# Kernel tuning notes

Hardware: AMD Instinct MI355X
Metric: run time of the kernel (lower is better)

## Reference

```python
import jax, jax.numpy as jnp
import numpy as np

N, E, D_IN, D_H, D_OUT = 100000, 1600000, 128, 128, 47
BN_EPS = 1e-5


def setup_inputs() -> dict:
    key = jax.random.key(0)
    ks = jax.random.split(key, 12)
    x = jax.random.normal(ks[0], (N, D_IN), dtype=jnp.float32)
    edge_index = jax.random.randint(ks[1], (2, E), 0, N, dtype=jnp.int64)
    s = 1.0 / np.sqrt(D_H)
    return {
        "x": x,
        "edge_index": edge_index,
        "W1": jax.random.normal(ks[2], (D_IN, D_H), dtype=jnp.float32) * s,
        "b1": jnp.zeros((D_H,), dtype=jnp.float32),
        "gamma": jax.random.uniform(ks[3], (D_H,), dtype=jnp.float32, minval=0.5, maxval=1.5),
        "beta": jax.random.normal(ks[4], (D_H,), dtype=jnp.float32) * 0.1,
        "mean": jax.random.normal(ks[5], (D_H,), dtype=jnp.float32) * 0.1,
        "var": jax.random.uniform(ks[6], (D_H,), dtype=jnp.float32, minval=0.5, maxval=1.5),
        "W2": jax.random.normal(ks[7], (D_H, D_H), dtype=jnp.float32) * s,
        "b2": jnp.zeros((D_H,), dtype=jnp.float32),
        "Wf": jax.random.normal(ks[8], (D_H, D_OUT), dtype=jnp.float32) * s,
        "bf": jnp.zeros((D_OUT,), dtype=jnp.float32),
    }


def gcn_conv(x, src, dst, W, b, n):
    # x' = x @ W, then symmetric-normalized aggregation with self-loops (PyG GCNConv).
    h = x @ W
    loops = jnp.arange(n, dtype=src.dtype)
    s = jnp.concatenate([src, loops])
    d = jnp.concatenate([dst, loops])
    deg = jax.ops.segment_sum(jnp.ones_like(d, dtype=h.dtype), d, num_segments=n)
    dinv = jnp.where(deg > 0, jax.lax.rsqrt(deg), 0.0)
    norm = dinv[s] * dinv[d]                      # [E+N]
    msg = h[s] * norm[:, None]                    # [E+N, D] gather
    out = jax.ops.segment_sum(msg, d, num_segments=n)  # scatter-add
    return out + b


def reference(x, edge_index, W1, b1, gamma, beta, mean, var, W2, b2, Wf, bf):
    n = x.shape[0]
    src, dst = edge_index[0], edge_index[1]
    # layer 1: GCNConv -> BatchNorm (eval) -> ReLU -> dropout (identity in eval)
    h1 = gcn_conv(x, src, dst, W1, b1, n)
    h1 = (h1 - mean) * jax.lax.rsqrt(var + BN_EPS) * gamma + beta
    h1 = jax.nn.relu(h1)
    # layer 2 (last conv, no BN/act)
    h2 = gcn_conv(h1, src, dst, W2, b2, n)
    # JumpingKnowledge max over layer outputs
    jk = jnp.maximum(h1, h2)
    logits = jk @ Wf + bf
    return jax.nn.log_softmax(logits, axis=1)
```

## Files before the change

kernel.cpp:

```cpp
#include <hip/hip_runtime.h>
#include <math.h>

#define DH 128
#define DOUT 47
#define BN_EPS 1e-5f

typedef __attribute__((ext_vector_type(8))) short short8;
typedef __attribute__((ext_vector_type(4))) float float4v;

__device__ __forceinline__ unsigned bf16_rne(float f) {
    unsigned u = __float_as_uint(f);
    return (u + 0x7fffu + ((u >> 16) & 1u)) >> 16;
}
__device__ __forceinline__ unsigned pack_bf2(float a, float b) {
    return (bf16_rne(a) & 0xffffu) | (bf16_rne(b) << 16);
}
__device__ __forceinline__ float2 unpack_bf2(unsigned u) {
    return make_float2(__uint_as_float(u << 16),
                       __uint_as_float(u & 0xffff0000u));
}


__global__ void zero_int_k(int* __restrict__ p, int n) {
    int i = blockIdx.x * 256 + threadIdx.x;
    if (i < n) p[i] = 0;
}

__global__ __launch_bounds__(256) void scan1_k(const int* __restrict__ counts,
                                               int* __restrict__ offsets,
                                               int* __restrict__ blocksums, int n) {
    __shared__ int sd[256];
    int tid = threadIdx.x;
    int base = blockIdx.x * 1024 + tid * 4;
    int v0 = (base + 0 < n) ? counts[base + 0] : 0;
    int v1 = (base + 1 < n) ? counts[base + 1] : 0;
    int v2 = (base + 2 < n) ? counts[base + 2] : 0;
    int v3 = (base + 3 < n) ? counts[base + 3] : 0;
    int tsum = v0 + v1 + v2 + v3;
    sd[tid] = tsum;
    __syncthreads();
    for (int off = 1; off < 256; off <<= 1) {
        int x = (tid >= off) ? sd[tid - off] : 0;
        __syncthreads();
        sd[tid] += x;
        __syncthreads();
    }
    if (tid == 255) blocksums[blockIdx.x] = sd[255];
    int run = sd[tid] - tsum;
    if (base + 0 < n) offsets[base + 0] = run;  run += v0;
    if (base + 1 < n) offsets[base + 1] = run;  run += v1;
    if (base + 2 < n) offsets[base + 2] = run;  run += v2;
    if (base + 3 < n) offsets[base + 3] = run;
}

__global__ __launch_bounds__(128) void scan2_k(int* __restrict__ blocksums, int nb) {
    __shared__ int sd[128];
    int tid = threadIdx.x;
    int v = (tid < nb) ? blocksums[tid] : 0;
    sd[tid] = v;
    __syncthreads();
    for (int off = 1; off < 128; off <<= 1) {
        int x = (tid >= off) ? sd[tid - off] : 0;
        __syncthreads();
        sd[tid] += x;
        __syncthreads();
    }
    if (tid < nb) blocksums[tid] = sd[tid] - v;
}

__global__ void finalize_k(int* __restrict__ offsets, int* __restrict__ cursor,
                           float* __restrict__ dinv, const int* __restrict__ counts,
                           const int* __restrict__ blocksums, int n) {
    int i = blockIdx.x * 256 + threadIdx.x;
    if (i >= n) return;
    int o = offsets[i] + blocksums[i >> 10];
    offsets[i] = o;
    cursor[i] = o;
    dinv[i] = rsqrtf((float)(counts[i] + 1));
}

__global__ void fill_k(const int* __restrict__ src, const int* __restrict__ dst,
                       const float* __restrict__ dinv, int* __restrict__ cursor,
                       int2* __restrict__ ew, int e, int n) {
    int i = blockIdx.x * 256 + threadIdx.x;
    int stride = gridDim.x * 256;
    for (; i < e; i += stride) {
        int d = dst[i];
        if ((unsigned)d < (unsigned)n) {
            int s = src[i];
            int pos = atomicAdd(&cursor[d], 1);
            int2 rec;
            rec.x = s;
            rec.y = __float_as_int(dinv[s] * dinv[d]);
            ew[pos] = rec;
        }
    }
}

__global__ __launch_bounds__(256) void wprep_k(const float* __restrict__ W1,
                                               const float* __restrict__ W2,
                                               unsigned* __restrict__ W1b,
                                               unsigned* __restrict__ W2b) {
    const float* W = blockIdx.x ? W2 : W1;
    unsigned* Wb = blockIdx.x ? W2b : W1b;
    int tid = threadIdx.x;
    for (int p = tid; p < 128 * 32; p += 256) {
        int n = p >> 5;
        int k0 = (p & 31) << 2;
        float f0 = W[(size_t)(k0 + 0) * 128 + n];
        float f1 = W[(size_t)(k0 + 1) * 128 + n];
        float f2 = W[(size_t)(k0 + 2) * 128 + n];
        float f3 = W[(size_t)(k0 + 3) * 128 + n];
        uint2 v;
        v.x = pack_bf2(f0, f1);
        v.y = pack_bf2(f2, f3);
        *(uint2*)(Wb + (size_t)n * 64 + (k0 >> 1)) = v;
    }
}

#define COUNT_BLOCKS 2048

__device__ __forceinline__ void gemm_mfma_body(const float* __restrict__ A,
                                               const unsigned* __restrict__ Wb,
                                               unsigned* __restrict__ Cb, int M,
                                               int blk) {
    __shared__ ushort Bl[128 * 136];
    int tid = threadIdx.x;
    {
        unsigned* Bu = (unsigned*)Bl;
        for (int q = tid; q < 128 * 16; q += 256) {
            int row = q >> 4;
            int c = (q & 15) << 2;
            uint4 v = *(const uint4*)(Wb + (size_t)row * 64 + c);
            *(uint4*)(Bu + (size_t)row * 68 + c) = v;
        }
    }
    __syncthreads();

    int lane = tid & 63;
    int wv = tid >> 6;
    int quad = lane >> 4;
    int l15 = lane & 15;
    int r0 = blk * 64 + wv * 16;
    int mload = r0 + l15;
    if (mload > M - 1) mload = M - 1;
    const float* Ar = A + (size_t)mload * 128 + quad * 8;

    float4v acc[8];
#pragma unroll
    for (int t = 0; t < 8; t++) acc[t] = (float4v){0.f, 0.f, 0.f, 0.f};

    for (int kp = 0; kp < 4; ++kp) {
        float4 a0 = *(const float4*)(Ar + kp * 32);
        float4 a1 = *(const float4*)(Ar + kp * 32 + 4);
        float af[8] = {a0.x, a0.y, a0.z, a0.w, a1.x, a1.y, a1.z, a1.w};
        short8 hi, lo;
#pragma unroll
        for (int j = 0; j < 8; j++) {
            unsigned h = bf16_rne(af[j]);
            hi[j] = (short)h;
            float res = af[j] - __uint_as_float(h << 16);
            lo[j] = (short)bf16_rne(res);
        }
        int kb = kp * 32 + quad * 8;
#pragma unroll
        for (int nt = 0; nt < 8; nt++) {
            short8 b8 = *(const short8*)(&Bl[(size_t)(nt * 16 + l15) * 136 + kb]);
            acc[nt] = __builtin_amdgcn_mfma_f32_16x16x32_bf16(hi, b8, acc[nt], 0, 0, 0);
            acc[nt] = __builtin_amdgcn_mfma_f32_16x16x32_bf16(lo, b8, acc[nt], 0, 0, 0);
        }
    }

    ushort* Cu = (ushort*)Cb;
#pragma unroll
    for (int r = 0; r < 4; r++) {
        int row = r0 + quad * 4 + r;
        if (row < M) {
#pragma unroll
            for (int nt = 0; nt < 8; nt++) {
                Cu[(size_t)row * 128 + nt * 16 + l15] = (ushort)bf16_rne(acc[nt][r]);
            }
        }
    }
}

__global__ __launch_bounds__(256) void gemm_mfma_k(const float* __restrict__ A,
                                                   const unsigned* __restrict__ Wb,
                                                   unsigned* __restrict__ Cb, int M) {
    gemm_mfma_body(A, Wb, Cb, M, blockIdx.x);
}

__global__ __launch_bounds__(256) void gemm1_count_k(
    const float* __restrict__ A, const unsigned* __restrict__ Wb,
    unsigned* __restrict__ Cb, int M, int gemmBlocks,
    const int* __restrict__ dst, int* __restrict__ counts, int e, int n) {
    if ((int)blockIdx.x >= gemmBlocks) {
        int bid = blockIdx.x - gemmBlocks;
        int i = bid * 256 + threadIdx.x;
        int stride = COUNT_BLOCKS * 256;
        for (; i < e; i += stride) {
            int d = dst[i];
            if ((unsigned)d < (unsigned)n) atomicAdd(&counts[d], 1);
        }
        return;
    }
    gemm_mfma_body(A, Wb, Cb, M, blockIdx.x);
}

__device__ __forceinline__ float2 agg_core(const unsigned* __restrict__ Hrow,
                                           const int2* __restrict__ ew,
                                           int start, int cnt, int node,
                                           int lane, float di) {
    float2 self = unpack_bf2(Hrow[(size_t)node * 64 + lane]);
    float wself = di * di;
    float2 acc = make_float2(self.x * wself, self.y * wself);
    if (cnt <= 0) return acc;

    const int2* ep = ew + start;
    int iters = (cnt + 3) >> 2;

    unsigned fC[4];
    float wC[4];
    int2 eN[4];
    {
        int2 e0[4];
#pragma unroll
        for (int k = 0; k < 4; k++) e0[k] = ep[k];
#pragma unroll
        for (int k = 0; k < 4; k++) {
            bool v = k < cnt;
            int s = v ? e0[k].x : 0;
            wC[k] = v ? __int_as_float(e0[k].y) : 0.f;
            fC[k] = Hrow[(size_t)s * 64 + lane];
        }
#pragma unroll
        for (int k = 0; k < 4; k++) eN[k] = ep[4 + k];
    }

    for (int g = 0; g < iters; ++g) {
        unsigned fN[4];
        float wN[4];
        int bN = (g + 1) << 2;
#pragma unroll
        for (int k = 0; k < 4; k++) {
            bool v = (bN + k) < cnt;
            int s = v ? eN[k].x : 0;
            wN[k] = v ? __int_as_float(eN[k].y) : 0.f;
            fN[k] = Hrow[(size_t)s * 64 + lane];
        }
#pragma unroll
        for (int k = 0; k < 4; k++) eN[k] = ep[bN + 4 + k];
#pragma unroll
        for (int k = 0; k < 4; k++) {
            float2 f = unpack_bf2(fC[k]);
            acc.x = fmaf(f.x, wC[k], acc.x);
            acc.y = fmaf(f.y, wC[k], acc.y);
        }
#pragma unroll
        for (int k = 0; k < 4; k++) { fC[k] = fN[k]; wC[k] = wN[k]; }
    }
    return acc;
}

__global__ __launch_bounds__(256) void agg1_k(
    const unsigned* __restrict__ H, const int2* __restrict__ ew,
    const int* __restrict__ offsets, const int* __restrict__ counts,
    const float* __restrict__ dinv, const float* __restrict__ b1,
    const float* __restrict__ gamma, const float* __restrict__ beta,
    const float* __restrict__ mean, const float* __restrict__ var,
    float* __restrict__ H1, int n) {
    int lane = threadIdx.x & 63;
    int node = blockIdx.x * 4 + (threadIdx.x >> 6);
    if (node >= n) return;
    float2 acc = agg_core(H, ew, offsets[node], counts[node],
                          node, lane, dinv[node]);
    int t0 = lane * 2;
    float2 bb = *(const float2*)(b1 + t0);
    float2 mm = *(const float2*)(mean + t0);
    float2 vv = *(const float2*)(var + t0);
    float2 gg = *(const float2*)(gamma + t0);
    float2 be = *(const float2*)(beta + t0);
    float vx = (acc.x + bb.x - mm.x) * rsqrtf(vv.x + BN_EPS) * gg.x + be.x;
    float vy = (acc.y + bb.y - mm.y) * rsqrtf(vv.y + BN_EPS) * gg.y + be.y;
    float2 outv = make_float2(fmaxf(vx, 0.f), fmaxf(vy, 0.f));
    *(float2*)(H1 + (size_t)node * 128 + t0) = outv;
}

__global__ __launch_bounds__(256) void agg2_k(
    const unsigned* __restrict__ H, const int2* __restrict__ ew,
    const int* __restrict__ offsets, const int* __restrict__ counts,
    const float* __restrict__ dinv, const float* __restrict__ b2,
    float* __restrict__ H1JK, int n) {
    int lane = threadIdx.x & 63;
    int node = blockIdx.x * 4 + (threadIdx.x >> 6);
    if (node >= n) return;
    float2 acc = agg_core(H, ew, offsets[node], counts[node],
                          node, lane, dinv[node]);
    int t0 = lane * 2;
    float2 bb = *(const float2*)(b2 + t0);
    float2* p = (float2*)(H1JK + (size_t)node * 128 + t0);
    float2 h1v = *p;
    float2 outv = make_float2(fmaxf(h1v.x, acc.x + bb.x),
                              fmaxf(h1v.y, acc.y + bb.y));
    *p = outv;
}

__global__ __launch_bounds__(256) void head_k(const float* __restrict__ JK,
                                              const float* __restrict__ Wf,
                                              const float* __restrict__ bf,
                                              float* __restrict__ out, int n) {
    __shared__ __align__(16) float Bs[48 * 132];
    __shared__ __align__(16) float As[64 * 36];
    int tid = threadIdx.x;
    for (int p = tid; p < 47 * 32; p += 256) {
        int c = p >> 5;
        int k0 = (p & 31) << 2;
        float4 v;
        v.x = Wf[(size_t)(k0 + 0) * DOUT + c];
        v.y = Wf[(size_t)(k0 + 1) * DOUT + c];
        v.z = Wf[(size_t)(k0 + 2) * DOUT + c];
        v.w = Wf[(size_t)(k0 + 3) * DOUT + c];
        *(float4*)(&Bs[c * 132 + k0]) = v;
    }
    int tx = tid & 15;
    int ty = tid >> 4;
    int node0 = blockIdx.x * 64;

    float acc[4][3];
#pragma unroll
    for (int i = 0; i < 4; i++)
#pragma unroll
        for (int j = 0; j < 3; j++) acc[i][j] = 0.f;

    for (int kk = 0; kk < 128; kk += 32) {
        __syncthreads();
        for (int l = tid; l < 512; l += 256) {
            int r = l >> 3;
            int c4 = (l & 7) << 2;
            int row = node0 + r;
            float4 v = make_float4(0.f, 0.f, 0.f, 0.f);
            if (row < n) v = *(const float4*)(JK + (size_t)row * 128 + kk + c4);
            *(float4*)(&As[r * 36 + c4]) = v;
        }
        __syncthreads();
#pragma unroll
        for (int k4 = 0; k4 < 32; k4 += 4) {
            float4 a0 = *(const float4*)(&As[(ty * 4 + 0) * 36 + k4]);
            float4 a1 = *(const float4*)(&As[(ty * 4 + 1) * 36 + k4]);
            float4 a2 = *(const float4*)(&As[(ty * 4 + 2) * 36 + k4]);
            float4 a3 = *(const float4*)(&As[(ty * 4 + 3) * 36 + k4]);
            float4 b0 = *(const float4*)(&Bs[(tx * 3 + 0) * 132 + kk + k4]);
            float4 b1 = *(const float4*)(&Bs[(tx * 3 + 1) * 132 + kk + k4]);
            float4 b2 = *(const float4*)(&Bs[(tx * 3 + 2) * 132 + kk + k4]);
#define DOT_ROW(i, a)                                                        \
            acc[i][0] = fmaf(a.x, b0.x, acc[i][0]);                          \
            acc[i][0] = fmaf(a.y, b0.y, acc[i][0]);                          \
            acc[i][0] = fmaf(a.z, b0.z, acc[i][0]);                          \
            acc[i][0] = fmaf(a.w, b0.w, acc[i][0]);                          \
            acc[i][1] = fmaf(a.x, b1.x, acc[i][1]);                          \
            acc[i][1] = fmaf(a.y, b1.y, acc[i][1]);                          \
            acc[i][1] = fmaf(a.z, b1.z, acc[i][1]);                          \
            acc[i][1] = fmaf(a.w, b1.w, acc[i][1]);                          \
            acc[i][2] = fmaf(a.x, b2.x, acc[i][2]);                          \
            acc[i][2] = fmaf(a.y, b2.y, acc[i][2]);                          \
            acc[i][2] = fmaf(a.z, b2.z, acc[i][2]);                          \
            acc[i][2] = fmaf(a.w, b2.w, acc[i][2]);
            DOT_ROW(0, a0)
            DOT_ROW(1, a1)
            DOT_ROW(2, a2)
            DOT_ROW(3, a3)
#undef DOT_ROW
        }
    }

    float bfv[3];
#pragma unroll
    for (int j = 0; j < 3; j++) {
        int c = tx * 3 + j;
        bfv[j] = (c < DOUT) ? bf[c] : 0.f;
    }
#pragma unroll
    for (int i = 0; i < 4; i++) {
        int node = node0 + ty * 4 + i;
        float l0 = acc[i][0] + bfv[0];
        float l1 = acc[i][1] + bfv[1];
        float l2 = acc[i][2] + bfv[2];
        bool v2ok = (tx * 3 + 2) < DOUT;
        float m = fmaxf(l0, l1);
        if (v2ok) m = fmaxf(m, l2);
        for (int off = 8; off >= 1; off >>= 1) m = fmaxf(m, __shfl_xor(m, off));
        float s = expf(l0 - m) + expf(l1 - m) + (v2ok ? expf(l2 - m) : 0.f);
        for (int off = 8; off >= 1; off >>= 1) s += __shfl_xor(s, off);
        float ls = m + logf(s);
        if (node < n) {
            float* o = out + (size_t)node * DOUT + tx * 3;
            o[0] = l0 - ls;
            o[1] = l1 - ls;
            if (v2ok) o[2] = l2 - ls;
        }
    }
}

extern "C" void kernel_launch(void* const* d_in, const int* in_sizes, int n_in,
                              void* d_out, int out_size, void* d_ws, size_t ws_size,
                              hipStream_t stream) {
    const float* x     = (const float*)d_in[0];
    const int*   ei    = (const int*)d_in[1];
    const float* W1    = (const float*)d_in[2];
    const float* b1    = (const float*)d_in[3];
    const float* gamma = (const float*)d_in[4];
    const float* beta  = (const float*)d_in[5];
    const float* mean  = (const float*)d_in[6];
    const float* var   = (const float*)d_in[7];
    const float* W2    = (const float*)d_in[8];
    const float* b2    = (const float*)d_in[9];
    const float* Wf    = (const float*)d_in[10];
    const float* bf    = (const float*)d_in[11];
    float* out = (float*)d_out;

    int N_ = in_sizes[0] / 128;
    int E_ = in_sizes[1] / 2;
    const int* src = ei;
    const int* dst = ei + E_;

    char* ws = (char*)d_ws;
    unsigned* bufA = (unsigned*)ws; ws += (size_t)N_ * 64 * 4;
    float* h1      = (float*)ws;  ws += (size_t)N_ * 128 * 4;
    int*   counts  = (int*)ws;    ws += (size_t)N_ * 4;
    int*   offsets = (int*)ws;    ws += (size_t)N_ * 4;
    int*   cursor  = (int*)ws;    ws += (size_t)N_ * 4;
    float* dinv    = (float*)ws;  ws += (size_t)N_ * 4;
    int2*  ew      = (int2*)ws;   ws += ((size_t)E_ + 16) * 8;
    int*   bsums   = (int*)ws;    ws += 1024 * 4;
    unsigned* W1b  = (unsigned*)ws; ws += 128 * 64 * 4;
    unsigned* W2b  = (unsigned*)ws; ws += 128 * 64 * 4;

    int nb = (N_ + 1023) / 1024;
    int gemmBlocks = (N_ + 63) / 64;

    zero_int_k<<<(N_ + 255) / 256, 256, 0, stream>>>(counts, N_);
    wprep_k<<<2, 256, 0, stream>>>(W1, W2, W1b, W2b);
    gemm1_count_k<<<gemmBlocks + COUNT_BLOCKS, 256, 0, stream>>>(
        x, W1b, bufA, N_, gemmBlocks, dst, counts, E_, N_);
    scan1_k<<<nb, 256, 0, stream>>>(counts, offsets, bsums, N_);
    scan2_k<<<1, 128, 0, stream>>>(bsums, nb);
    finalize_k<<<(N_ + 255) / 256, 256, 0, stream>>>(offsets, cursor, dinv, counts, bsums, N_);
    fill_k<<<2048, 256, 0, stream>>>(src, dst, dinv, cursor, ew, E_, N_);

    agg1_k<<<(N_ + 3) / 4, 256, 0, stream>>>(bufA, ew, offsets, counts, dinv,
                                             b1, gamma, beta, mean, var, h1, N_);
    gemm_mfma_k<<<gemmBlocks, 256, 0, stream>>>(h1, W2b, bufA, N_);
    agg2_k<<<(N_ + 3) / 4, 256, 0, stream>>>(bufA, ew, offsets, counts, dinv,
                                             b2, h1, N_);
    head_k<<<(N_ + 63) / 64, 256, 0, stream>>>(h1, Wf, bf, out, N_);
}
```

Baseline: 506.0 us.

## Pad CSR rows to multiples of 8 and split wave into two 8-byte-lane halves

Each node's edge list in the CSR is padded to a multiple of 8 with zero-weight records, written in finalize_k, so the aggregation loop needs no bounds masks. The aggregation wave is split into two 32-lane halves: each lane loads 8 bytes (4 bf16 features) per neighbor, and the halves work on alternating edges before combining with a cross-half shuffle. This aims to issue wider gathers and keep more neighbor rows in flight per wave. In exchange the edge array grows by up to 7 records per node, and the padded records still cost gather traffic (they read row 0).

```diff
diff --git a/kernel.cpp b/kernel.cpp
--- a/kernel.cpp
+++ b/kernel.cpp
@@ -32,10 +32,10 @@
     __shared__ int sd[256];
     int tid = threadIdx.x;
     int base = blockIdx.x * 1024 + tid * 4;
-    int v0 = (base + 0 < n) ? counts[base + 0] : 0;
-    int v1 = (base + 1 < n) ? counts[base + 1] : 0;
-    int v2 = (base + 2 < n) ? counts[base + 2] : 0;
-    int v3 = (base + 3 < n) ? counts[base + 3] : 0;
+    int v0 = (base + 0 < n) ? ((counts[base + 0] + 7) & ~7) : 0;
+    int v1 = (base + 1 < n) ? ((counts[base + 1] + 7) & ~7) : 0;
+    int v2 = (base + 2 < n) ? ((counts[base + 2] + 7) & ~7) : 0;
+    int v3 = (base + 3 < n) ? ((counts[base + 3] + 7) & ~7) : 0;
     int tsum = v0 + v1 + v2 + v3;
     sd[tid] = tsum;
     __syncthreads();
@@ -70,13 +70,18 @@
 
 __global__ void finalize_k(int* __restrict__ offsets, int* __restrict__ cursor,
                            float* __restrict__ dinv, const int* __restrict__ counts,
-                           const int* __restrict__ blocksums, int n) {
+                           const int* __restrict__ blocksums,
+                           int2* __restrict__ ew, int n) {
     int i = blockIdx.x * 256 + threadIdx.x;
     if (i >= n) return;
     int o = offsets[i] + blocksums[i >> 10];
     offsets[i] = o;
     cursor[i] = o;
-    dinv[i] = rsqrtf((float)(counts[i] + 1));
+    int c = counts[i];
+    dinv[i] = rsqrtf((float)(c + 1));
+    int cP = (c + 7) & ~7;
+    int2 z; z.x = 0; z.y = 0;
+    for (int j = o + c; j < o + cP; ++j) ew[j] = z;
 }
 
 __global__ void fill_k(const int* __restrict__ src, const int* __restrict__ dst,
@@ -207,58 +212,52 @@
     gemm_mfma_body(A, Wb, Cb, M, blockIdx.x);
 }
 
-__device__ __forceinline__ float2 agg_core(const unsigned* __restrict__ Hrow,
+__device__ __forceinline__ float4 agg_core(const uint2* __restrict__ Hu2,
                                            const int2* __restrict__ ew,
                                            int start, int cnt, int node,
-                                           int lane, float di) {
-    float2 self = unpack_bf2(Hrow[(size_t)node * 64 + lane]);
-    float wself = di * di;
-    float2 acc = make_float2(self.x * wself, self.y * wself);
-    if (cnt <= 0) return acc;
-
-    const int2* ep = ew + start;
-    int iters = (cnt + 3) >> 2;
-
-    unsigned fC[4];
-    float wC[4];
-    int2 eN[4];
-    {
-        int2 e0[4];
-#pragma unroll
-        for (int k = 0; k < 4; k++) e0[k] = ep[k];
-#pragma unroll
-        for (int k = 0; k < 4; k++) {
-            bool v = k < cnt;
-            int s = v ? e0[k].x : 0;
-            wC[k] = v ? __int_as_float(e0[k].y) : 0.f;
-            fC[k] = Hrow[(size_t)s * 64 + lane];
-        }
-#pragma unroll
-        for (int k = 0; k < 4; k++) eN[k] = ep[4 + k];
-    }
-
-    for (int g = 0; g < iters; ++g) {
-        unsigned fN[4];
-        float wN[4];
-        int bN = (g + 1) << 2;
-#pragma unroll
-        for (int k = 0; k < 4; k++) {
-            bool v = (bN + k) < cnt;
-            int s = v ? eN[k].x : 0;
-            wN[k] = v ? __int_as_float(eN[k].y) : 0.f;
-            fN[k] = Hrow[(size_t)s * 64 + lane];
-        }
-#pragma unroll
-        for (int k = 0; k < 4; k++) eN[k] = ep[bN + 4 + k];
-#pragma unroll
-        for (int k = 0; k < 4; k++) {
-            float2 f = unpack_bf2(fC[k]);
-            acc.x = fmaf(f.x, wC[k], acc.x);
-            acc.y = fmaf(f.y, wC[k], acc.y);
-        }
-#pragma unroll
-        for (int k = 0; k < 4; k++) { fC[k] = fN[k]; wC[k] = wN[k]; }
-    }
+                                           int li, int half, float di) {
+    float4 acc = make_float4(0.f, 0.f, 0.f, 0.f);
+    int groups = ((cnt + 7) & ~7) >> 3;
+    if (groups > 0) {
+        const int2* p = ew + start + half;
+        int2 r[4];
+#pragma unroll
+        for (int k = 0; k < 4; k++) r[k] = p[2 * k];
+        for (int g = 0; g < groups; ++g) {
+            uint2 gb[4];
+#pragma unroll
+            for (int k = 0; k < 4; k++)
+                gb[k] = Hu2[(size_t)r[k].x * 32 + li];
+            int2 rn[4];
+            const int2* pn = p + 8 * (g + 1);
+#pragma unroll
+            for (int k = 0; k < 4; k++) rn[k] = pn[2 * k];
+#pragma unroll
+            for (int k = 0; k < 4; k++) {
+                float w = __int_as_float(r[k].y);
+                float2 f0 = unpack_bf2(gb[k].x);
+                float2 f1 = unpack_bf2(gb[k].y);
+                acc.x = fmaf(f0.x, w, acc.x);
+                acc.y = fmaf(f0.y, w, acc.y);
+                acc.z = fmaf(f1.x, w, acc.z);
+                acc.w = fmaf(f1.y, w, acc.w);
+            }
+#pragma unroll
+            for (int k = 0; k < 4; k++) r[k] = rn[k];
+        }
+    }
+    acc.x += __shfl_xor(acc.x, 32);
+    acc.y += __shfl_xor(acc.y, 32);
+    acc.z += __shfl_xor(acc.z, 32);
+    acc.w += __shfl_xor(acc.w, 32);
+    uint2 sv = Hu2[(size_t)node * 32 + li];
+    float ws = di * di;
+    float2 s0 = unpack_bf2(sv.x);
+    float2 s1 = unpack_bf2(sv.y);
+    acc.x = fmaf(s0.x, ws, acc.x);
+    acc.y = fmaf(s0.y, ws, acc.y);
+    acc.z = fmaf(s1.x, ws, acc.z);
+    acc.w = fmaf(s1.y, ws, acc.w);
     return acc;
 }
 
@@ -270,20 +269,26 @@
     const float* __restrict__ mean, const float* __restrict__ var,
     float* __restrict__ H1, int n) {
     int lane = threadIdx.x & 63;
+    int li = lane & 31;
+    int half = lane >> 5;
     int node = blockIdx.x * 4 + (threadIdx.x >> 6);
     if (node >= n) return;
-    float2 acc = agg_core(H, ew, offsets[node], counts[node],
-                          node, lane, dinv[node]);
-    int t0 = lane * 2;
-    float2 bb = *(const float2*)(b1 + t0);
-    float2 mm = *(const float2*)(mean + t0);
-    float2 vv = *(const float2*)(var + t0);
-    float2 gg = *(const float2*)(gamma + t0);
-    float2 be = *(const float2*)(beta + t0);
-    float vx = (acc.x + bb.x - mm.x) * rsqrtf(vv.x + BN_EPS) * gg.x + be.x;
-    float vy = (acc.y + bb.y - mm.y) * rsqrtf(vv.y + BN_EPS) * gg.y + be.y;
-    float2 outv = make_float2(fmaxf(vx, 0.f), fmaxf(vy, 0.f));
-    *(float2*)(H1 + (size_t)node * 128 + t0) = outv;
+    float4 acc = agg_core((const uint2*)H, ew, offsets[node], counts[node],
+                          node, li, half, dinv[node]);
+    if (half == 0) {
+        int f0 = li * 4;
+        float4 bb = *(const float4*)(b1 + f0);
+        float4 mm = *(const float4*)(mean + f0);
+        float4 vv = *(const float4*)(var + f0);
+        float4 gg = *(const float4*)(gamma + f0);
+        float4 be = *(const float4*)(beta + f0);
+        float4 o;
+        o.x = fmaxf((acc.x + bb.x - mm.x) * rsqrtf(vv.x + BN_EPS) * gg.x + be.x, 0.f);
+        o.y = fmaxf((acc.y + bb.y - mm.y) * rsqrtf(vv.y + BN_EPS) * gg.y + be.y, 0.f);
+        o.z = fmaxf((acc.z + bb.z - mm.z) * rsqrtf(vv.z + BN_EPS) * gg.z + be.z, 0.f);
+        o.w = fmaxf((acc.w + bb.w - mm.w) * rsqrtf(vv.w + BN_EPS) * gg.w + be.w, 0.f);
+        *(float4*)(H1 + (size_t)node * 128 + f0) = o;
+    }
 }
 
 __global__ __launch_bounds__(256) void agg2_k(
@@ -292,17 +297,24 @@
     const float* __restrict__ dinv, const float* __restrict__ b2,
     float* __restrict__ H1JK, int n) {
     int lane = threadIdx.x & 63;
+    int li = lane & 31;
+    int half = lane >> 5;
     int node = blockIdx.x * 4 + (threadIdx.x >> 6);
     if (node >= n) return;
-    float2 acc = agg_core(H, ew, offsets[node], counts[node],
-                          node, lane, dinv[node]);
-    int t0 = lane * 2;
-    float2 bb = *(const float2*)(b2 + t0);
-    float2* p = (float2*)(H1JK + (size_t)node * 128 + t0);
-    float2 h1v = *p;
-    float2 outv = make_float2(fmaxf(h1v.x, acc.x + bb.x),
-                              fmaxf(h1v.y, acc.y + bb.y));
-    *p = outv;
+    float4 acc = agg_core((const uint2*)H, ew, offsets[node], counts[node],
+                          node, li, half, dinv[node]);
+    if (half == 0) {
+        int f0 = li * 4;
+        float4 bb = *(const float4*)(b2 + f0);
+        float4* p = (float4*)(H1JK + (size_t)node * 128 + f0);
+        float4 h1v = *p;
+        float4 o;
+        o.x = fmaxf(h1v.x, acc.x + bb.x);
+        o.y = fmaxf(h1v.y, acc.y + bb.y);
+        o.z = fmaxf(h1v.z, acc.z + bb.z);
+        o.w = fmaxf(h1v.w, acc.w + bb.w);
+        *p = o;
+    }
 }
 
 __global__ __launch_bounds__(256) void head_k(const float* __restrict__ JK,
@@ -430,7 +442,7 @@
     int*   offsets = (int*)ws;    ws += (size_t)N_ * 4;
     int*   cursor  = (int*)ws;    ws += (size_t)N_ * 4;
     float* dinv    = (float*)ws;  ws += (size_t)N_ * 4;
-    int2*  ew      = (int2*)ws;   ws += ((size_t)E_ + 16) * 8;
+    int2*  ew      = (int2*)ws;   ws += ((size_t)E_ + 7 * (size_t)N_ + 64) * 8;
     int*   bsums   = (int*)ws;    ws += 1024 * 4;
     unsigned* W1b  = (unsigned*)ws; ws += 128 * 64 * 4;
     unsigned* W2b  = (unsigned*)ws; ws += 128 * 64 * 4;
@@ -444,7 +456,8 @@
         x, W1b, bufA, N_, gemmBlocks, dst, counts, E_, N_);
     scan1_k<<<nb, 256, 0, stream>>>(counts, offsets, bsums, N_);
     scan2_k<<<1, 128, 0, stream>>>(bsums, nb);
-    finalize_k<<<(N_ + 255) / 256, 256, 0, stream>>>(offsets, cursor, dinv, counts, bsums, N_);
+    finalize_k<<<(N_ + 255) / 256, 256, 0, stream>>>(offsets, cursor, dinv,
+                                                     counts, bsums, ew, N_);
     fill_k<<<2048, 256, 0, stream>>>(src, dst, dinv, cursor, ew, E_, N_);
 
     agg1_k<<<(N_ + 3) / 4, 256, 0, stream>>>(bufA, ew, offsets, counts, dinv,
```

Result: no change. 507.6 us (+0.3%).
